# Kernel tuning notes

Measured on AMD Instinct MI355X. Metric: run time of the kernel, lower is better.

Reference implementation:

```python
import jax, jax.numpy as jnp
import numpy as np

B, S, E, H = 2, 4096, 512, 8
D = E // H


def setup_inputs() -> dict:
    key = jax.random.key(0)
    ks = jax.random.split(key, 6)
    x = jax.random.normal(ks[0], (B, S, E), dtype=jnp.float32)
    scale = E ** -0.5
    in_proj_w = jax.random.normal(ks[1], (3 * E, E), dtype=jnp.float32) * scale
    in_proj_b = jnp.zeros((3 * E,), dtype=jnp.float32)
    out_proj_w = jax.random.normal(ks[2], (E, E), dtype=jnp.float32) * scale
    out_proj_b = jnp.zeros((E,), dtype=jnp.float32)
    t = jax.random.normal(ks[3], (H,), dtype=jnp.float32)
    return {"x": x, "in_proj_w": in_proj_w, "in_proj_b": in_proj_b,
            "out_proj_w": out_proj_w, "out_proj_b": out_proj_b, "t": t}


def reference(x, in_proj_w, in_proj_b, out_proj_w, out_proj_b, t):
    b, s, e = x.shape
    h, d = H, D
    # packed qkv projection as in nn.MultiheadAttention
    qkv = x @ in_proj_w.T + in_proj_b              # [b, s, 3e]
    q, k, v = jnp.split(qkv, 3, axis=-1)
    q = q.reshape(b, s, h, d).transpose(0, 2, 1, 3)  # [b, h, s, d]
    k = k.reshape(b, s, h, d).transpose(0, 2, 1, 3)
    v = v.reshape(b, s, h, d).transpose(0, 2, 1, 3)
    scores = jnp.einsum("bhqd,bhkd->bhqk", q, k) / jnp.sqrt(jnp.float32(d))
    # Gaussian relative-position bias: -(j-k)^2 / (2 * (t^2)^2), per head
    idx = jnp.arange(s)
    dist2 = (idx[None, :] - idx[:, None]).astype(jnp.float32) ** 2  # [s, s]
    sigma = t ** 2                                                  # [h]
    bias = -dist2[None, :, :] / (2.0 * (sigma ** 2)[:, None, None]) # [h, s, s]
    attn = jax.nn.softmax(scores + bias[None], axis=-1)             # [b, h, s, s]
    out = jnp.einsum("bhqk,bhkd->bhqd", attn, v)                    # [b, h, s, d]
    out = out.transpose(0, 2, 1, 3).reshape(b, s, e)
    return out @ out_proj_w.T + out_proj_b
```

## Files before the change

### kernel.cpp

```cpp
#include <hip/hip_runtime.h>
#include <hip/hip_bf16.h>
#include <stdint.h>

#define LOG2E 1.4426950408889634f

typedef __bf16 bf16;
typedef __bf16 bf16x8 __attribute__((ext_vector_type(8)));
typedef float  f32x4  __attribute__((ext_vector_type(4)));

__device__ __forceinline__ f32x4 mfma16(bf16x8 a, bf16x8 b, f32x4 c) {
    return __builtin_amdgcn_mfma_f32_16x16x32_bf16(a, b, c, 0, 0, 0);
}

__device__ __forceinline__ void async16(const void* g, void* l) {
    __builtin_amdgcn_global_load_lds(
        (const __attribute__((address_space(1))) void*)g,
        (__attribute__((address_space(3))) void*)l, 16, 0, 0);
}

__global__ __launch_bounds__(256) void cvt_kernel(
    const float* __restrict__ X, const float* __restrict__ Wi,
    const float* __restrict__ Wo,
    bf16* __restrict__ Xb, bf16* __restrict__ Wib, bf16* __restrict__ Wob)
{
    size_t e = ((size_t)blockIdx.x * 256 + threadIdx.x) * 8;
    const float* src; bf16* dst; size_t off;
    if (e < 4194304)      { src = X;  dst = Xb;  off = e; }
    else if (e < 4980736) { src = Wi; dst = Wib; off = e - 4194304; }
    else                  { src = Wo; dst = Wob; off = e - 4980736; }
    float4 f0 = *(const float4*)(src + off);
    float4 f1 = *(const float4*)(src + off + 4);
    bf16x8 v = { (bf16)f0.x,(bf16)f0.y,(bf16)f0.z,(bf16)f0.w,
                 (bf16)f1.x,(bf16)f1.y,(bf16)f1.z,(bf16)f1.w };
    *(bf16x8*)(dst + off) = v;
}

__global__ __launch_bounds__(256) void qkv_gemm_kernel(
    const bf16* __restrict__ Xb, const bf16* __restrict__ Wb,
    const float* __restrict__ bias,
    bf16* __restrict__ Qb, bf16* __restrict__ Kb, bf16* __restrict__ Vt)
{
    const int tid  = threadIdx.x;
    const int lane = tid & 63;
    const int wv   = tid >> 6;
    const int quad = lane >> 4;
    const int ln   = lane & 15;
    const int bm   = blockIdx.x;
    const int bn   = blockIdx.y;

    __shared__ __align__(16) bf16 As[128 * 64];
    __shared__ __align__(16) bf16 Bs[128 * 64];

    const int wm = (wv >> 1) * 64;
    const int wn = (wv & 1) * 64;

    const int srow = tid >> 3;
    const int scc  = tid & 7;

    const bf16* XA = Xb + (size_t)bm * 128 * 512;
    const bf16* WB = Wb + (size_t)bn * 128 * 512;

    f32x4 acc[4][4] = {};

    for (int kt = 0; kt < 512; kt += 64) {
        #pragma unroll
        for (int i = 0; i < 4; ++i) {
            int c   = tid + 256 * i;
            int row = srow + 32 * i;
            int cg  = scc ^ (row & 7);
            async16(XA + (size_t)row * 512 + kt + cg * 8, As + c * 8);
            async16(WB + (size_t)row * 512 + kt + cg * 8, Bs + c * 8);
        }
        __syncthreads();

        bf16x8 af[4][2], bfr[4][2];
        #pragma unroll
        for (int i = 0; i < 4; ++i) {
            #pragma unroll
            for (int c = 0; c < 2; ++c) {
                int ra = wm + i * 16 + ln;
                af[i][c]  = *(const bf16x8*)&As[(ra * 8 + ((c * 4 + quad) ^ (ra & 7))) * 8];
                int rb = wn + i * 16 + ln;
                bfr[i][c] = *(const bf16x8*)&Bs[(rb * 8 + ((c * 4 + quad) ^ (rb & 7))) * 8];
            }
        }
        #pragma unroll
        for (int c = 0; c < 2; ++c)
            #pragma unroll
            for (int i = 0; i < 4; ++i)
                #pragma unroll
                for (int j = 0; j < 4; ++j)
                    acc[i][j] = mfma16(af[i][c], bfr[j][c], acc[i][j]);
        __syncthreads();
    }

    #pragma unroll
    for (int i = 0; i < 4; ++i) {
        int mbase = bm * 128 + wm + i * 16 + quad * 4;
        #pragma unroll
        for (int j = 0; j < 4; ++j) {
            int n = bn * 128 + wn + j * 16 + ln;
            float bv = bias[n];
            int sec = n >> 9;
            int e = n & 511;
            int hh = e >> 6, dd = e & 63;
            #pragma unroll
            for (int r = 0; r < 4; ++r) {
                int mm = mbase + r;
                int b = mm >> 12, s = mm & 4095;
                bf16 v = (bf16)(acc[i][j][r] + bv);
                size_t bhi = (size_t)(b * 8 + hh);
                if (sec == 0)      Qb[(bhi * 4096 + s) * 64 + dd] = v;
                else if (sec == 1) Kb[(bhi * 4096 + s) * 64 + dd] = v;
                else               Vt[(bhi * 64 + dd) * 4096 + s] = v;
            }
        }
    }
}

__global__ __launch_bounds__(256) void attn_kernel(
    const bf16* __restrict__ Qb, const bf16* __restrict__ Kb,
    const bf16* __restrict__ Vt, const float* __restrict__ T,
    bf16* __restrict__ AO)
{
    const int tid  = threadIdx.x;
    const int lane = tid & 63;
    const int wv   = tid >> 6;
    const int quad = lane >> 4;
    const int ln   = lane & 15;
    const int qt   = blockIdx.x;
    const int bh   = blockIdx.y;
    const int h    = bh & 7;
    const int b    = bh >> 3;

    __shared__ __align__(16) bf16 KVs[2][2][64 * 64];
    __shared__ __align__(16) bf16 Ps[4][16 * 64];

    const float t  = T[h];
    const float s2 = t * t;
    const float cb = 1.0f / (2.0f * s2 * s2);

    const int R  = (int)ceilf(s2 * 8.0f) + 1;
    int lo = qt * 64 - R;      if (lo < 0) lo = 0;     lo &= ~63;
    int hi = qt * 64 + 64 + R; if (hi > 4096) hi = 4096; hi = (hi + 63) & ~63;

    const float c1  = 0.125f * LOG2E;
    const float c2m = -cb * LOG2E;
    const float c3m = -12.0f * LOG2E;

    const int qrow_f = qt * 64 + wv * 16 + ln;
    const bf16* qptr = Qb + ((size_t)bh * 4096 + qrow_f) * 64 + quad * 8;
    bf16x8 qf0 = *(const bf16x8*)qptr;
    bf16x8 qf1 = *(const bf16x8*)(qptr + 32);

    const int qrow_c = qt * 64 + wv * 16 + quad * 4;
    const float fln = (float)ln;

    f32x4 o[4] = {};
    f32x4 lsum = {};
    const bf16 one = (bf16)1.0f;
    const bf16x8 onesv = { one, one, one, one, one, one, one, one };

    const int srow = tid >> 3;
    const int scc  = tid & 7;

    for (int ct = lo; ct < hi; ct += 128) {
        const int ntiles = ((hi - ct) >= 128) ? 2 : 1;
        __syncthreads();
        #pragma unroll
        for (int tt = 0; tt < 2; ++tt) {
            if (tt < ntiles) {
                const bf16* Kg = Kb + ((size_t)bh * 4096 + ct + tt * 64) * 64;
                const bf16* Vg = Vt + (size_t)bh * 64 * 4096 + ct + tt * 64;
                bf16* Ksl = &KVs[tt][0][0];
                bf16* Vsl = &KVs[tt][1][0];
                #pragma unroll
                for (int i = 0; i < 2; ++i) {
                    int c = tid + 256 * i;
                    int row = srow + 32 * i;
                    int cg = scc ^ (row & 7);
                    async16(Kg + row * 64 + cg * 8, Ksl + c * 8);
                    async16(Vg + (size_t)row * 4096 + cg * 8, Vsl + c * 8);
                }
            }
        }
        __syncthreads();

        for (int tt = 0; tt < ntiles; ++tt) {
            const int kt = ct + tt * 64;
            const bf16* Ks = &KVs[tt][0][0];
            const bf16* Vs = &KVs[tt][1][0];

            f32x4 sc[4] = {};
            #pragma unroll
            for (int tI = 0; tI < 4; ++tI) {
                int row = tI * 16 + ln;
                bf16x8 kf0 = *(const bf16x8*)&Ks[(row * 8 + ((quad    ) ^ (row & 7))) * 8];
                bf16x8 kf1 = *(const bf16x8*)&Ks[(row * 8 + ((4 + quad) ^ (row & 7))) * 8];
                sc[tI] = mfma16(qf0, kf0, sc[tI]);
                sc[tI] = mfma16(qf1, kf1, sc[tI]);
            }

            float p[4][4];
            #pragma unroll
            for (int r = 0; r < 4; ++r) {
                float Ar = (float)(qrow_c + r - kt) - fln;
                #pragma unroll
                for (int tI = 0; tI < 4; ++tI) {
                    float df = Ar - (float)(tI * 16);
                    float lg = fmaf(sc[tI][r], c1, fmaf(df, df * c2m, c3m));
                    p[tI][r] = __builtin_amdgcn_exp2f(lg);
                }
            }

            #pragma unroll
            for (int tI = 0; tI < 4; ++tI)
                #pragma unroll
                for (int r = 0; r < 4; ++r) {
                    int row = quad * 4 + r;
                    int cc  = tI * 2 + (ln >> 3);
                    int idx = row * 64 + ((cc ^ (row & 7)) * 8) + (ln & 7);
                    Ps[wv][idx] = (bf16)p[tI][r];
                }

            bf16x8 pf[2];
            #pragma unroll
            for (int c = 0; c < 2; ++c)
                pf[c] = *(const bf16x8*)&Ps[wv][(ln * 8 + ((c * 4 + quad) ^ (ln & 7))) * 8];

            #pragma unroll
            for (int c = 0; c < 2; ++c)
                lsum = mfma16(pf[c], onesv, lsum);
            #pragma unroll
            for (int t2 = 0; t2 < 4; ++t2) {
                int vrow = t2 * 16 + ln;
                #pragma unroll
                for (int c = 0; c < 2; ++c) {
                    bf16x8 vf = *(const bf16x8*)&Vs[(vrow * 8 + ((c * 4 + quad) ^ (vrow & 7))) * 8];
                    o[t2] = mfma16(pf[c], vf, o[t2]);
                }
            }
        }
    }

    float il[4];
    #pragma unroll
    for (int r = 0; r < 4; ++r) il[r] = __builtin_amdgcn_rcpf(lsum[r]);
    #pragma unroll
    for (int t2 = 0; t2 < 4; ++t2) {
        int dd = t2 * 16 + ln;
        #pragma unroll
        for (int r = 0; r < 4; ++r) {
            int s = qt * 64 + wv * 16 + quad * 4 + r;
            AO[((size_t)(b * 4096 + s)) * 512 + h * 64 + dd] = (bf16)(o[t2][r] * il[r]);
        }
    }
}

__global__ __launch_bounds__(256) void out_gemm_kernel(
    const bf16* __restrict__ A, const bf16* __restrict__ Wb,
    const float* __restrict__ bias, float* __restrict__ OUT)
{
    const int tid  = threadIdx.x;
    const int lane = tid & 63;
    const int wv   = tid >> 6;
    const int quad = lane >> 4;
    const int ln   = lane & 15;
    const int bm   = blockIdx.x;
    const int bn   = blockIdx.y;

    __shared__ __align__(16) bf16 As[128 * 64];
    __shared__ __align__(16) bf16 Bs[128 * 64];

    const int wm = (wv >> 1) * 64;
    const int wn = (wv & 1) * 64;

    const int srow = tid >> 3;
    const int scc  = tid & 7;

    const bf16* AA = A  + (size_t)bm * 128 * 512;
    const bf16* WB = Wb + (size_t)bn * 128 * 512;

    f32x4 acc[4][4] = {};

    for (int kt = 0; kt < 512; kt += 64) {
        #pragma unroll
        for (int i = 0; i < 4; ++i) {
            int c   = tid + 256 * i;
            int row = srow + 32 * i;
            int cg  = scc ^ (row & 7);
            async16(AA + (size_t)row * 512 + kt + cg * 8, As + c * 8);
            async16(WB + (size_t)row * 512 + kt + cg * 8, Bs + c * 8);
        }
        __syncthreads();

        bf16x8 af[4][2], bfr[4][2];
        #pragma unroll
        for (int i = 0; i < 4; ++i) {
            #pragma unroll
            for (int c = 0; c < 2; ++c) {
                int ra = wm + i * 16 + ln;
                af[i][c]  = *(const bf16x8*)&As[(ra * 8 + ((c * 4 + quad) ^ (ra & 7))) * 8];
                int rb = wn + i * 16 + ln;
                bfr[i][c] = *(const bf16x8*)&Bs[(rb * 8 + ((c * 4 + quad) ^ (rb & 7))) * 8];
            }
        }
        #pragma unroll
        for (int c = 0; c < 2; ++c)
            #pragma unroll
            for (int i = 0; i < 4; ++i)
                #pragma unroll
                for (int j = 0; j < 4; ++j)
                    acc[i][j] = mfma16(af[i][c], bfr[j][c], acc[i][j]);
        __syncthreads();
    }

    #pragma unroll
    for (int i = 0; i < 4; ++i) {
        int mbase = bm * 128 + wm + i * 16 + quad * 4;
        #pragma unroll
        for (int j = 0; j < 4; ++j) {
            int n = bn * 128 + wn + j * 16 + ln;
            float bv = bias[n];
            #pragma unroll
            for (int r = 0; r < 4; ++r)
                OUT[(size_t)(mbase + r) * 512 + n] = acc[i][j][r] + bv;
        }
    }
}

extern "C" void kernel_launch(void* const* d_in, const int* in_sizes, int n_in,
                              void* d_out, int out_size, void* d_ws, size_t ws_size,
                              hipStream_t stream)
{
    const float* x  = (const float*)d_in[0];
    const float* wi = (const float*)d_in[1];
    const float* bi = (const float*)d_in[2];
    const float* wo = (const float*)d_in[3];
    const float* bo = (const float*)d_in[4];
    const float* t  = (const float*)d_in[5];
    float* out = (float*)d_out;

    bf16* Qb  = (bf16*)d_ws;
    bf16* Kb  = Qb  + 4194304;
    bf16* Vt  = Kb  + 4194304;
    bf16* AO  = Vt  + 4194304;
    bf16* Xb  = AO  + 4194304;
    bf16* Wib = Xb  + 4194304;
    bf16* Wob = Wib + 786432;

    cvt_kernel     <<<dim3(2560), 256, 0, stream>>>(x, wi, wo, Xb, Wib, Wob);
    qkv_gemm_kernel<<<dim3(64, 12), 256, 0, stream>>>(Xb, Wib, bi, Qb, Kb, Vt);
    attn_kernel    <<<dim3(64, 16), 256, 0, stream>>>(Qb, Kb, Vt, t, AO);
    out_gemm_kernel<<<dim3(64, 4), 256, 0, stream>>>(AO, Wob, bo, out);
}
```

Measured before the change: 126.3 us.

## Fuse all four stages into one persistent kernel with grid-wide barriers

Merges the conversion, QKV GEMM, attention and output GEMM kernels into one persistent kernel of 512 blocks. The blocks loop over each stage's tiles and separate stages with atomic-counter grid barriers. This removes three kernel launch gaps and the pipeline drain between stages. In exchange it adds a memset launch, spin-wait barriers and load imbalance from the fixed block count. It also relies on all 512 blocks being co-resident, or the barriers deadlock.

```diff
diff --git a/kernel.cpp b/kernel.cpp
--- a/kernel.cpp
+++ b/kernel.cpp
@@ -3,6 +3,7 @@
 #include <stdint.h>
 
 #define LOG2E 1.4426950408889634f
+#define NBLK 512
 
 typedef __bf16 bf16;
 typedef __bf16 bf16x8 __attribute__((ext_vector_type(8)));
@@ -18,313 +19,315 @@
         (__attribute__((address_space(3))) void*)l, 16, 0, 0);
 }
 
-__global__ __launch_bounds__(256) void cvt_kernel(
-    const float* __restrict__ X, const float* __restrict__ Wi,
-    const float* __restrict__ Wo,
-    bf16* __restrict__ Xb, bf16* __restrict__ Wib, bf16* __restrict__ Wob)
+__device__ __forceinline__ void gbar(unsigned int* bar) {
+    __syncthreads();
+    if (threadIdx.x == 0) {
+        __threadfence();
+        __hip_atomic_fetch_add(bar, 1u, __ATOMIC_ACQ_REL, __HIP_MEMORY_SCOPE_AGENT);
+        while (__hip_atomic_load(bar, __ATOMIC_ACQUIRE, __HIP_MEMORY_SCOPE_AGENT)
+               != (unsigned int)NBLK)
+            __builtin_amdgcn_s_sleep(4);
+        __threadfence();
+    }
+    __syncthreads();
+}
+
+__global__ __launch_bounds__(256, 2) void fused_kernel(
+    const float* __restrict__ X,  const float* __restrict__ Wi,
+    const float* __restrict__ Bi, const float* __restrict__ Wo,
+    const float* __restrict__ Bo, const float* __restrict__ T,
+    float* OUT, bf16* WS, unsigned int* BAR)
 {
-    size_t e = ((size_t)blockIdx.x * 256 + threadIdx.x) * 8;
-    const float* src; bf16* dst; size_t off;
-    if (e < 4194304)      { src = X;  dst = Xb;  off = e; }
-    else if (e < 4980736) { src = Wi; dst = Wib; off = e - 4194304; }
-    else                  { src = Wo; dst = Wob; off = e - 4980736; }
-    float4 f0 = *(const float4*)(src + off);
-    float4 f1 = *(const float4*)(src + off + 4);
-    bf16x8 v = { (bf16)f0.x,(bf16)f0.y,(bf16)f0.z,(bf16)f0.w,
-                 (bf16)f1.x,(bf16)f1.y,(bf16)f1.z,(bf16)f1.w };
-    *(bf16x8*)(dst + off) = v;
-}
-
-__global__ __launch_bounds__(256) void qkv_gemm_kernel(
-    const bf16* __restrict__ Xb, const bf16* __restrict__ Wb,
-    const float* __restrict__ bias,
-    bf16* __restrict__ Qb, bf16* __restrict__ Kb, bf16* __restrict__ Vt)
-{
+    __shared__ __align__(16) bf16 SMEM[20480];
+
+    bf16* Qb  = WS;
+    bf16* Kb  = Qb + 4194304;
+    bf16* Vt  = Kb + 4194304;
+    bf16* AO  = Vt + 4194304;
+    bf16* Xb  = AO + 4194304;
+    bf16* Wib = Xb + 4194304;
+    bf16* Wob = Wib + 786432;
+
     const int tid  = threadIdx.x;
+    const int blk  = blockIdx.x;
     const int lane = tid & 63;
     const int wv   = tid >> 6;
     const int quad = lane >> 4;
     const int ln   = lane & 15;
-    const int bm   = blockIdx.x;
-    const int bn   = blockIdx.y;
-
-    __shared__ __align__(16) bf16 As[128 * 64];
-    __shared__ __align__(16) bf16 Bs[128 * 64];
-
-    const int wm = (wv >> 1) * 64;
-    const int wn = (wv & 1) * 64;
-
     const int srow = tid >> 3;
     const int scc  = tid & 7;
 
-    const bf16* XA = Xb + (size_t)bm * 128 * 512;
-    const bf16* WB = Wb + (size_t)bn * 128 * 512;
-
-    f32x4 acc[4][4] = {};
-
-    for (int kt = 0; kt < 512; kt += 64) {
-        #pragma unroll
-        for (int i = 0; i < 4; ++i) {
-            int c   = tid + 256 * i;
-            int row = srow + 32 * i;
-            int cg  = scc ^ (row & 7);
-            async16(XA + (size_t)row * 512 + kt + cg * 8, As + c * 8);
-            async16(WB + (size_t)row * 512 + kt + cg * 8, Bs + c * 8);
+    for (size_t c = (size_t)blk * 256 + tid; c < 655360; c += (size_t)NBLK * 256) {
+        size_t e = c * 8;
+        const float* src; bf16* dst; size_t off;
+        if (e < 4194304)      { src = X;  dst = Xb;  off = e; }
+        else if (e < 4980736) { src = Wi; dst = Wib; off = e - 4194304; }
+        else                  { src = Wo; dst = Wob; off = e - 4980736; }
+        float4 f0 = *(const float4*)(src + off);
+        float4 f1 = *(const float4*)(src + off + 4);
+        bf16x8 v = { (bf16)f0.x,(bf16)f0.y,(bf16)f0.z,(bf16)f0.w,
+                     (bf16)f1.x,(bf16)f1.y,(bf16)f1.z,(bf16)f1.w };
+        *(bf16x8*)(dst + off) = v;
+    }
+    gbar(BAR + 0);
+
+    {
+        bf16* As = SMEM;
+        bf16* Bs = SMEM + 8192;
+        const int wm = (wv >> 1) * 64;
+        const int wn = (wv & 1) * 64;
+
+        for (int tl = blk; tl < 768; tl += NBLK) {
+            const int bm = tl & 63, bn = tl >> 6;
+            const bf16* XA = Xb  + (size_t)bm * 128 * 512;
+            const bf16* WB = Wib + (size_t)bn * 128 * 512;
+
+            f32x4 acc[4][4] = {};
+
+            for (int kt = 0; kt < 512; kt += 64) {
+                #pragma unroll
+                for (int i = 0; i < 4; ++i) {
+                    int c   = tid + 256 * i;
+                    int row = srow + 32 * i;
+                    int cg2 = scc ^ (row & 7);
+                    async16(XA + (size_t)row * 512 + kt + cg2 * 8, As + c * 8);
+                    async16(WB + (size_t)row * 512 + kt + cg2 * 8, Bs + c * 8);
+                }
+                __syncthreads();
+
+                bf16x8 af[4][2], bfr[4][2];
+                #pragma unroll
+                for (int i = 0; i < 4; ++i) {
+                    #pragma unroll
+                    for (int c = 0; c < 2; ++c) {
+                        int ra = wm + i * 16 + ln;
+                        af[i][c]  = *(const bf16x8*)&As[(ra * 8 + ((c * 4 + quad) ^ (ra & 7))) * 8];
+                        int rb = wn + i * 16 + ln;
+                        bfr[i][c] = *(const bf16x8*)&Bs[(rb * 8 + ((c * 4 + quad) ^ (rb & 7))) * 8];
+                    }
+                }
+                #pragma unroll
+                for (int c = 0; c < 2; ++c)
+                    #pragma unroll
+                    for (int i = 0; i < 4; ++i)
+                        #pragma unroll
+                        for (int j = 0; j < 4; ++j)
+                            acc[i][j] = mfma16(af[i][c], bfr[j][c], acc[i][j]);
+                __syncthreads();
+            }
+
+            #pragma unroll
+            for (int i = 0; i < 4; ++i) {
+                int mbase = bm * 128 + wm + i * 16 + quad * 4;
+                #pragma unroll
+                for (int j = 0; j < 4; ++j) {
+                    int n = bn * 128 + wn + j * 16 + ln;
+                    float bv = Bi[n];
+                    int sec = n >> 9;
+                    int e = n & 511;
+                    int hh = e >> 6, dd = e & 63;
+                    #pragma unroll
+                    for (int r = 0; r < 4; ++r) {
+                        int mm = mbase + r;
+                        int b = mm >> 12, s = mm & 4095;
+                        bf16 v = (bf16)(acc[i][j][r] + bv);
+                        size_t bhi = (size_t)(b * 8 + hh);
+                        if (sec == 0)      Qb[(bhi * 4096 + s) * 64 + dd] = v;
+                        else if (sec == 1) Kb[(bhi * 4096 + s) * 64 + dd] = v;
+                        else               Vt[(bhi * 64 + dd) * 4096 + s] = v;
+                    }
+                }
+            }
         }
-        __syncthreads();
-
-        bf16x8 af[4][2], bfr[4][2];
-        #pragma unroll
-        for (int i = 0; i < 4; ++i) {
+    }
+    gbar(BAR + 1);
+
+    {
+        const float c1 = 0.125f * LOG2E;
+
+        for (int tl = blk; tl < 1024; tl += NBLK) {
+            const int qt = tl & 63;
+            const int bh = tl >> 6;
+            const int h  = bh & 7;
+            const int b  = bh >> 3;
+
+            const float t  = T[h];
+            const float s2 = t * t;
+            const float cb = 1.0f / (2.0f * s2 * s2);
+
+            const int R  = (int)ceilf(s2 * 8.0f) + 1;
+            int lo = qt * 64 - R;      if (lo < 0) lo = 0;     lo &= ~63;
+            int hi = qt * 64 + 64 + R; if (hi > 4096) hi = 4096; hi = (hi + 63) & ~63;
+
+            const float c2m = -cb * LOG2E;
+            const float c3m = -12.0f * LOG2E;
+
+            const int qrow_f = qt * 64 + wv * 16 + ln;
+            const bf16* qptr = Qb + ((size_t)bh * 4096 + qrow_f) * 64 + quad * 8;
+            bf16x8 qf0 = *(const bf16x8*)qptr;
+            bf16x8 qf1 = *(const bf16x8*)(qptr + 32);
+
+            const int qrow_c = qt * 64 + wv * 16 + quad * 4;
+            const float fln = (float)ln;
+
+            f32x4 o[4] = {};
+            f32x4 lsum = {};
+            const bf16 one = (bf16)1.0f;
+            const bf16x8 onesv = { one, one, one, one, one, one, one, one };
+
+            for (int ct = lo; ct < hi; ct += 128) {
+                const int ntiles = ((hi - ct) >= 128) ? 2 : 1;
+                __syncthreads();
+                #pragma unroll
+                for (int tt = 0; tt < 2; ++tt) {
+                    if (tt < ntiles) {
+                        const bf16* Kg = Kb + ((size_t)bh * 4096 + ct + tt * 64) * 64;
+                        const bf16* Vg = Vt + (size_t)bh * 64 * 4096 + ct + tt * 64;
+                        bf16* Ksl = SMEM + (tt * 2 + 0) * 4096;
+                        bf16* Vsl = SMEM + (tt * 2 + 1) * 4096;
+                        #pragma unroll
+                        for (int i = 0; i < 2; ++i) {
+                            int c = tid + 256 * i;
+                            int row = srow + 32 * i;
+                            int cg2 = scc ^ (row & 7);
+                            async16(Kg + row * 64 + cg2 * 8, Ksl + c * 8);
+                            async16(Vg + (size_t)row * 4096 + cg2 * 8, Vsl + c * 8);
+                        }
+                    }
+                }
+                __syncthreads();
+
+                for (int tt = 0; tt < ntiles; ++tt) {
+                    const int kt = ct + tt * 64;
+                    const bf16* Ks = SMEM + tt * 8192;
+                    const bf16* Vs = Ks + 4096;
+                    bf16* Pw = SMEM + 16384 + wv * 1024;
+
+                    f32x4 sc[4] = {};
+                    #pragma unroll
+                    for (int tI = 0; tI < 4; ++tI) {
+                        int row = tI * 16 + ln;
+                        bf16x8 kf0 = *(const bf16x8*)&Ks[(row * 8 + ((quad    ) ^ (row & 7))) * 8];
+                        bf16x8 kf1 = *(const bf16x8*)&Ks[(row * 8 + ((4 + quad) ^ (row & 7))) * 8];
+                        sc[tI] = mfma16(qf0, kf0, sc[tI]);
+                        sc[tI] = mfma16(qf1, kf1, sc[tI]);
+                    }
+
+                    float p[4][4];
+                    #pragma unroll
+                    for (int r = 0; r < 4; ++r) {
+                        float Ar = (float)(qrow_c + r - kt) - fln;
+                        #pragma unroll
+                        for (int tI = 0; tI < 4; ++tI) {
+                            float df = Ar - (float)(tI * 16);
+                            float lg = fmaf(sc[tI][r], c1, fmaf(df, df * c2m, c3m));
+                            p[tI][r] = __builtin_amdgcn_exp2f(lg);
+                        }
+                    }
+
+                    #pragma unroll
+                    for (int tI = 0; tI < 4; ++tI)
+                        #pragma unroll
+                        for (int r = 0; r < 4; ++r) {
+                            int row = quad * 4 + r;
+                            int cc  = tI * 2 + (ln >> 3);
+                            int idx = row * 64 + ((cc ^ (row & 7)) * 8) + (ln & 7);
+                            Pw[idx] = (bf16)p[tI][r];
+                        }
+
+                    bf16x8 pf[2];
+                    #pragma unroll
+                    for (int c = 0; c < 2; ++c)
+                        pf[c] = *(const bf16x8*)&Pw[(ln * 8 + ((c * 4 + quad) ^ (ln & 7))) * 8];
+
+                    #pragma unroll
+                    for (int c = 0; c < 2; ++c)
+                        lsum = mfma16(pf[c], onesv, lsum);
+                    #pragma unroll
+                    for (int t2 = 0; t2 < 4; ++t2) {
+                        int vrow = t2 * 16 + ln;
+                        #pragma unroll
+                        for (int c = 0; c < 2; ++c) {
+                            bf16x8 vf = *(const bf16x8*)&Vs[(vrow * 8 + ((c * 4 + quad) ^ (vrow & 7))) * 8];
+                            o[t2] = mfma16(pf[c], vf, o[t2]);
+                        }
+                    }
+                }
+            }
+
+            float il[4];
             #pragma unroll
-            for (int c = 0; c < 2; ++c) {
-                int ra = wm + i * 16 + ln;
-                af[i][c]  = *(const bf16x8*)&As[(ra * 8 + ((c * 4 + quad) ^ (ra & 7))) * 8];
-                int rb = wn + i * 16 + ln;
-                bfr[i][c] = *(const bf16x8*)&Bs[(rb * 8 + ((c * 4 + quad) ^ (rb & 7))) * 8];
-            }
-        }
-        #pragma unroll
-        for (int c = 0; c < 2; ++c)
-            #pragma unroll
-            for (int i = 0; i < 4; ++i)
-                #pragma unroll
-                for (int j = 0; j < 4; ++j)
-                    acc[i][j] = mfma16(af[i][c], bfr[j][c], acc[i][j]);
-        __syncthreads();
-    }
-
-    #pragma unroll
-    for (int i = 0; i < 4; ++i) {
-        int mbase = bm * 128 + wm + i * 16 + quad * 4;
-        #pragma unroll
-        for (int j = 0; j < 4; ++j) {
-            int n = bn * 128 + wn + j * 16 + ln;
-            float bv = bias[n];
-            int sec = n >> 9;
-            int e = n & 511;
-            int hh = e >> 6, dd = e & 63;
-            #pragma unroll
-            for (int r = 0; r < 4; ++r) {
-                int mm = mbase + r;
-                int b = mm >> 12, s = mm & 4095;
-                bf16 v = (bf16)(acc[i][j][r] + bv);
-                size_t bhi = (size_t)(b * 8 + hh);
-                if (sec == 0)      Qb[(bhi * 4096 + s) * 64 + dd] = v;
-                else if (sec == 1) Kb[(bhi * 4096 + s) * 64 + dd] = v;
-                else               Vt[(bhi * 64 + dd) * 4096 + s] = v;
-            }
-        }
-    }
-}
-
-__global__ __launch_bounds__(256) void attn_kernel(
-    const bf16* __restrict__ Qb, const bf16* __restrict__ Kb,
-    const bf16* __restrict__ Vt, const float* __restrict__ T,
-    bf16* __restrict__ AO)
-{
-    const int tid  = threadIdx.x;
-    const int lane = tid & 63;
-    const int wv   = tid >> 6;
-    const int quad = lane >> 4;
-    const int ln   = lane & 15;
-    const int qt   = blockIdx.x;
-    const int bh   = blockIdx.y;
-    const int h    = bh & 7;
-    const int b    = bh >> 3;
-
-    __shared__ __align__(16) bf16 KVs[2][2][64 * 64];
-    __shared__ __align__(16) bf16 Ps[4][16 * 64];
-
-    const float t  = T[h];
-    const float s2 = t * t;
-    const float cb = 1.0f / (2.0f * s2 * s2);
-
-    const int R  = (int)ceilf(s2 * 8.0f) + 1;
-    int lo = qt * 64 - R;      if (lo < 0) lo = 0;     lo &= ~63;
-    int hi = qt * 64 + 64 + R; if (hi > 4096) hi = 4096; hi = (hi + 63) & ~63;
-
-    const float c1  = 0.125f * LOG2E;
-    const float c2m = -cb * LOG2E;
-    const float c3m = -12.0f * LOG2E;
-
-    const int qrow_f = qt * 64 + wv * 16 + ln;
-    const bf16* qptr = Qb + ((size_t)bh * 4096 + qrow_f) * 64 + quad * 8;
-    bf16x8 qf0 = *(const bf16x8*)qptr;
-    bf16x8 qf1 = *(const bf16x8*)(qptr + 32);
-
-    const int qrow_c = qt * 64 + wv * 16 + quad * 4;
-    const float fln = (float)ln;
-
-    f32x4 o[4] = {};
-    f32x4 lsum = {};
-    const bf16 one = (bf16)1.0f;
-    const bf16x8 onesv = { one, one, one, one, one, one, one, one };
-
-    const int srow = tid >> 3;
-    const int scc  = tid & 7;
-
-    for (int ct = lo; ct < hi; ct += 128) {
-        const int ntiles = ((hi - ct) >= 128) ? 2 : 1;
-        __syncthreads();
-        #pragma unroll
-        for (int tt = 0; tt < 2; ++tt) {
-            if (tt < ntiles) {
-                const bf16* Kg = Kb + ((size_t)bh * 4096 + ct + tt * 64) * 64;
-                const bf16* Vg = Vt + (size_t)bh * 64 * 4096 + ct + tt * 64;
-                bf16* Ksl = &KVs[tt][0][0];
-                bf16* Vsl = &KVs[tt][1][0];
-                #pragma unroll
-                for (int i = 0; i < 2; ++i) {
-                    int c = tid + 256 * i;
-                    int row = srow + 32 * i;
-                    int cg = scc ^ (row & 7);
-                    async16(Kg + row * 64 + cg * 8, Ksl + c * 8);
-                    async16(Vg + (size_t)row * 4096 + cg * 8, Vsl + c * 8);
-                }
-            }
-        }
-        __syncthreads();
-
-        for (int tt = 0; tt < ntiles; ++tt) {
-            const int kt = ct + tt * 64;
-            const bf16* Ks = &KVs[tt][0][0];
-            const bf16* Vs = &KVs[tt][1][0];
-
-            f32x4 sc[4] = {};
-            #pragma unroll
-            for (int tI = 0; tI < 4; ++tI) {
-                int row = tI * 16 + ln;
-                bf16x8 kf0 = *(const bf16x8*)&Ks[(row * 8 + ((quad    ) ^ (row & 7))) * 8];
-                bf16x8 kf1 = *(const bf16x8*)&Ks[(row * 8 + ((4 + quad) ^ (row & 7))) * 8];
-                sc[tI] = mfma16(qf0, kf0, sc[tI]);
-                sc[tI] = mfma16(qf1, kf1, sc[tI]);
-            }
-
-            float p[4][4];
-            #pragma unroll
-            for (int r = 0; r < 4; ++r) {
-                float Ar = (float)(qrow_c + r - kt) - fln;
-                #pragma unroll
-                for (int tI = 0; tI < 4; ++tI) {
-                    float df = Ar - (float)(tI * 16);
-                    float lg = fmaf(sc[tI][r], c1, fmaf(df, df * c2m, c3m));
-                    p[tI][r] = __builtin_amdgcn_exp2f(lg);
-                }
-            }
-
-            #pragma unroll
-            for (int tI = 0; tI < 4; ++tI)
-                #pragma unroll
-                for (int r = 0; r < 4; ++r) {
-                    int row = quad * 4 + r;
-                    int cc  = tI * 2 + (ln >> 3);
-                    int idx = row * 64 + ((cc ^ (row & 7)) * 8) + (ln & 7);
-                    Ps[wv][idx] = (bf16)p[tI][r];
-                }
-
-            bf16x8 pf[2];
-            #pragma unroll
-            for (int c = 0; c < 2; ++c)
-                pf[c] = *(const bf16x8*)&Ps[wv][(ln * 8 + ((c * 4 + quad) ^ (ln & 7))) * 8];
-
-            #pragma unroll
-            for (int c = 0; c < 2; ++c)
-                lsum = mfma16(pf[c], onesv, lsum);
+            for (int r = 0; r < 4; ++r) il[r] = __builtin_amdgcn_rcpf(lsum[r]);
             #pragma unroll
             for (int t2 = 0; t2 < 4; ++t2) {
-                int vrow = t2 * 16 + ln;
-                #pragma unroll
-                for (int c = 0; c < 2; ++c) {
-                    bf16x8 vf = *(const bf16x8*)&Vs[(vrow * 8 + ((c * 4 + quad) ^ (vrow & 7))) * 8];
-                    o[t2] = mfma16(pf[c], vf, o[t2]);
+                int dd = t2 * 16 + ln;
+                #pragma unroll
+                for (int r = 0; r < 4; ++r) {
+                    int s = qt * 64 + wv * 16 + quad * 4 + r;
+                    AO[((size_t)(b * 4096 + s)) * 512 + h * 64 + dd] = (bf16)(o[t2][r] * il[r]);
                 }
             }
         }
     }
-
-    float il[4];
-    #pragma unroll
-    for (int r = 0; r < 4; ++r) il[r] = __builtin_amdgcn_rcpf(lsum[r]);
-    #pragma unroll
-    for (int t2 = 0; t2 < 4; ++t2) {
-        int dd = t2 * 16 + ln;
-        #pragma unroll
-        for (int r = 0; r < 4; ++r) {
-            int s = qt * 64 + wv * 16 + quad * 4 + r;
-            AO[((size_t)(b * 4096 + s)) * 512 + h * 64 + dd] = (bf16)(o[t2][r] * il[r]);
-        }
-    }
-}
-
-__global__ __launch_bounds__(256) void out_gemm_kernel(
-    const bf16* __restrict__ A, const bf16* __restrict__ Wb,
-    const float* __restrict__ bias, float* __restrict__ OUT)
-{
-    const int tid  = threadIdx.x;
-    const int lane = tid & 63;
-    const int wv   = tid >> 6;
-    const int quad = lane >> 4;
-    const int ln   = lane & 15;
-    const int bm   = blockIdx.x;
-    const int bn   = blockIdx.y;
-
-    __shared__ __align__(16) bf16 As[128 * 64];
-    __shared__ __align__(16) bf16 Bs[128 * 64];
-
-    const int wm = (wv >> 1) * 64;
-    const int wn = (wv & 1) * 64;
-
-    const int srow = tid >> 3;
-    const int scc  = tid & 7;
-
-    const bf16* AA = A  + (size_t)bm * 128 * 512;
-    const bf16* WB = Wb + (size_t)bn * 128 * 512;
-
-    f32x4 acc[4][4] = {};
-
-    for (int kt = 0; kt < 512; kt += 64) {
-        #pragma unroll
-        for (int i = 0; i < 4; ++i) {
-            int c   = tid + 256 * i;
-            int row = srow + 32 * i;
-            int cg  = scc ^ (row & 7);
-            async16(AA + (size_t)row * 512 + kt + cg * 8, As + c * 8);
-            async16(WB + (size_t)row * 512 + kt + cg * 8, Bs + c * 8);
-        }
-        __syncthreads();
-
-        bf16x8 af[4][2], bfr[4][2];
-        #pragma unroll
-        for (int i = 0; i < 4; ++i) {
+    gbar(BAR + 2);
+
+    {
+        bf16* As = SMEM;
+        bf16* Bs = SMEM + 8192;
+        const int wm = (wv >> 1) * 64;
+        const int wn = (wv & 1) * 64;
+
+        for (int tl = blk; tl < 256; tl += NBLK) {
+            const int bm = tl & 63, bn = tl >> 6;
+            const bf16* AA = AO  + (size_t)bm * 128 * 512;
+            const bf16* WB = Wob + (size_t)bn * 128 * 512;
+
+            f32x4 acc[4][4] = {};
+
+            for (int kt = 0; kt < 512; kt += 64) {
+                #pragma unroll
+                for (int i = 0; i < 4; ++i) {
+                    int c   = tid + 256 * i;
+                    int row = srow + 32 * i;
+                    int cg2 = scc ^ (row & 7);
+                    async16(AA + (size_t)row * 512 + kt + cg2 * 8, As + c * 8);
+                    async16(WB + (size_t)row * 512 + kt + cg2 * 8, Bs + c * 8);
+                }
+                __syncthreads();
+
+                bf16x8 af[4][2], bfr[4][2];
+                #pragma unroll
+                for (int i = 0; i < 4; ++i) {
+                    #pragma unroll
+                    for (int c = 0; c < 2; ++c) {
+                        int ra = wm + i * 16 + ln;
+                        af[i][c]  = *(const bf16x8*)&As[(ra * 8 + ((c * 4 + quad) ^ (ra & 7))) * 8];
+                        int rb = wn + i * 16 + ln;
+                        bfr[i][c] = *(const bf16x8*)&Bs[(rb * 8 + ((c * 4 + quad) ^ (rb & 7))) * 8];
+                    }
+                }
+                #pragma unroll
+                for (int c = 0; c < 2; ++c)
+                    #pragma unroll
+                    for (int i = 0; i < 4; ++i)
+                        #pragma unroll
+                        for (int j = 0; j < 4; ++j)
+                            acc[i][j] = mfma16(af[i][c], bfr[j][c], acc[i][j]);
+                __syncthreads();
+            }
+
             #pragma unroll
-            for (int c = 0; c < 2; ++c) {
-                int ra = wm + i * 16 + ln;
-                af[i][c]  = *(const bf16x8*)&As[(ra * 8 + ((c * 4 + quad) ^ (ra & 7))) * 8];
-                int rb = wn + i * 16 + ln;
-                bfr[i][c] = *(const bf16x8*)&Bs[(rb * 8 + ((c * 4 + quad) ^ (rb & 7))) * 8];
-            }
-        }
-        #pragma unroll
-        for (int c = 0; c < 2; ++c)
-            #pragma unroll
-            for (int i = 0; i < 4; ++i)
-                #pragma unroll
-                for (int j = 0; j < 4; ++j)
-                    acc[i][j] = mfma16(af[i][c], bfr[j][c], acc[i][j]);
-        __syncthreads();
-    }
-
-    #pragma unroll
-    for (int i = 0; i < 4; ++i) {
-        int mbase = bm * 128 + wm + i * 16 + quad * 4;
-        #pragma unroll
-        for (int j = 0; j < 4; ++j) {
-            int n = bn * 128 + wn + j * 16 + ln;
-            float bv = bias[n];
-            #pragma unroll
-            for (int r = 0; r < 4; ++r)
-                OUT[(size_t)(mbase + r) * 512 + n] = acc[i][j][r] + bv;
+            for (int i = 0; i < 4; ++i) {
+                int mbase = bm * 128 + wm + i * 16 + quad * 4;
+                #pragma unroll
+                for (int j = 0; j < 4; ++j) {
+                    int n = bn * 128 + wn + j * 16 + ln;
+                    float bv = Bo[n];
+                    #pragma unroll
+                    for (int r = 0; r < 4; ++r)
+                        OUT[(size_t)(mbase + r) * 512 + n] = acc[i][j][r] + bv;
+                }
+            }
         }
     }
 }
@@ -340,17 +343,11 @@
     const float* bo = (const float*)d_in[4];
     const float* t  = (const float*)d_in[5];
     float* out = (float*)d_out;
-
-    bf16* Qb  = (bf16*)d_ws;
-    bf16* Kb  = Qb  + 4194304;
-    bf16* Vt  = Kb  + 4194304;
-    bf16* AO  = Vt  + 4194304;
-    bf16* Xb  = AO  + 4194304;
-    bf16* Wib = Xb  + 4194304;
-    bf16* Wob = Wib + 786432;
-
-    cvt_kernel     <<<dim3(2560), 256, 0, stream>>>(x, wi, wo, Xb, Wib, Wob);
-    qkv_gemm_kernel<<<dim3(64, 12), 256, 0, stream>>>(Xb, Wib, bi, Qb, Kb, Vt);
-    attn_kernel    <<<dim3(64, 16), 256, 0, stream>>>(Qb, Kb, Vt, t, AO);
-    out_gemm_kernel<<<dim3(64, 4), 256, 0, stream>>>(AO, Wob, bo, out);
-}
+    bf16* ws   = (bf16*)d_ws;
+
+    unsigned int* bar = (unsigned int*)((char*)d_ws + (size_t)192 * 1024 * 1024);
+    hipMemsetAsync(bar, 0, 16, stream);
+
+    fused_kernel<<<dim3(NBLK), dim3(256), 0, stream>>>(
+        x, wi, bi, wo, bo, t, out, ws, bar);
+}
```

After: 359.4 us. 185% more time.
